# Performance work log

Measured on AMD Instinct MI355X. Metric: run time of the kernel, lower is better.

The kernel has to match this reference:

```python
import jax, jax.numpy as jnp
import numpy as np

B, C, K, D = 8192, 64, 256, 64  # batch, ncodebooks, ncentroids, subvect_len
BN_EPS = 1e-5


def setup_inputs() -> dict:
    key = jax.random.key(0)
    k1, k2 = jax.random.split(key)
    return {
        "inputs": jax.random.normal(k1, (B, C, D), dtype=jnp.float32),
        "centroids_k": jax.random.normal(k2, (C, K, D), dtype=jnp.float32) * 0.1,
        "bn_gamma": jnp.ones((C,), dtype=jnp.float32),
        "bn_beta": jnp.zeros((C,), dtype=jnp.float32),
    }


def _response(inputs, centroids_k, bn_gamma, bn_beta):
    # dot-metric scores: (B, C, K)
    r = jnp.einsum('bcd,ckd->bck', inputs, centroids_k)
    # BatchNorm1d over channel dim C (training mode: biased batch stats over B and K)
    mean = r.mean(axis=(0, 2), keepdims=True)
    var = ((r - mean) ** 2).mean(axis=(0, 2), keepdims=True)
    r = (r - mean) * jax.lax.rsqrt(var + BN_EPS)
    return r * bn_gamma[None, :, None] + bn_beta[None, :, None]


def reference(inputs, centroids_k, bn_gamma, bn_beta):
    r = _response(inputs, centroids_k, bn_gamma, bn_beta)
    # torch.max(response, -1) -> (values, indices)
    mse = r.max(axis=-1)                 # (B, C)
    codes = jnp.argmax(r, axis=-1)       # (B, C) int
    # tie_in_n_out=True: _centroids_v is _centroids_k
    return codes, mse, centroids_k
```

## Files before the change

kernel.cpp:

```cpp
#include <hip/hip_runtime.h>

#define B_  8192
#define C_  64
#define K_  256
#define D_  64
#define NBT     2
#define ROWS_BT 512
#define GX  (B_ / (ROWS_BT * NBT))
#define BC_ (B_ * C_)
#define BN_EPS 1e-5

#define WCAP_C 1024
#define DELTA  2.5e-3f

typedef _Float16 f16x8 __attribute__((ext_vector_type(8)));
typedef float    f32x4 __attribute__((ext_vector_type(4)));

__device__ __forceinline__ int swz(int row, int dbyte) {
    return (row * 128 + dbyte) ^ ((row & 7) << 4);
}

__device__ __forceinline__ f16x8 cvt8(const float* p) {
    float4 u0 = *(const float4*)p;
    float4 u1 = *(const float4*)(p + 4);
    return (f16x8){(_Float16)u0.x, (_Float16)u0.y, (_Float16)u0.z, (_Float16)u0.w,
                   (_Float16)u1.x, (_Float16)u1.y, (_Float16)u1.z, (_Float16)u1.w};
}

#define MERGE2(B1, S1, B2, S2)                                              \
    {                                                                       \
        const float lo_ = fminf(B1, B2);                                    \
        B1 = fmaxf(B1, B2);                                                 \
        S1 = fmaxf(lo_, fmaxf(S1, S2));                                     \
    }

__global__ __launch_bounds__(64) void dpq_prep(
    const float* __restrict__ cent, float* __restrict__ csum,
    int* __restrict__ wcount)
{
    const int c = blockIdx.x, d = threadIdx.x;
    const float* g = cent + (size_t)c * K_ * D_ + d;
    float s = 0.f;
#pragma unroll 8
    for (int k = 0; k < K_; ++k) s += g[(size_t)k * D_];
    csum[c * D_ + d] = s;
    if (d == 0) wcount[c] = 0;
}

__global__ __launch_bounds__(512, 4) void dpq_mfma(
    const float* __restrict__ x,
    const float* __restrict__ cent,
    const float* __restrict__ gamma,
    const float* __restrict__ csum,
    float* __restrict__ out,
    float* __restrict__ part_sum,
    float* __restrict__ part_sq,
    int* __restrict__ wcount,
    int* __restrict__ worklist)
{
    __shared__ char lds[34816];
    const int c   = blockIdx.y;
    const int tid = threadIdx.x;
    const float sgn = (gamma[c] < 0.0f) ? -1.0f : 1.0f;

    {
        const int row = tid >> 1, half = tid & 1;
        const float* g = cent + ((size_t)c * K_ + row) * D_ + half * 32;
#pragma unroll
        for (int q = 0; q < 4; ++q) {
            float v[8];
#pragma unroll
            for (int j = 0; j < 8; ++j) v[j] = g[q * 8 + j] * sgn;
            f16x8 h = {(_Float16)v[0], (_Float16)v[1], (_Float16)v[2], (_Float16)v[3],
                       (_Float16)v[4], (_Float16)v[5], (_Float16)v[6], (_Float16)v[7]};
            *(f16x8*)(lds + swz(row, half * 64 + q * 16)) = h;
        }
    }
    if (tid < 128) {
        const int row = tid >> 3, q = tid & 7;
        f16x8 h = {0, 0, 0, 0, 0, 0, 0, 0};
        if (row == 0) {
            const float* cs = csum + c * D_ + q * 8;
#pragma unroll
            for (int j = 0; j < 8; ++j) h[j] = (_Float16)(cs[j] * sgn);
        }
        *(f16x8*)(lds + 32768 + swz(row, q * 16)) = h;
    }
    __syncthreads();

    const int wid = tid >> 6, lane = tid & 63;
    const int col = lane & 15, grp = lane >> 4;
    const unsigned g4 = (unsigned)(grp * 4);

    float taccs[4] = {0.f, 0.f, 0.f, 0.f};
    float taccq[4] = {0.f, 0.f, 0.f, 0.f};

    for (int bt = 0; bt < NBT; ++bt) {
        const int b0 = blockIdx.x * (ROWS_BT * NBT) + bt * ROWS_BT + wid * 64;

        f16x8 xfa[4], xfb[4];
        {
            const float* xb = x + ((size_t)(b0 + col) * C_ + c) * D_ + grp * 8;
            const size_t st16 = (size_t)16 * C_ * D_;
#pragma unroll
            for (int T = 0; T < 4; ++T) {
                xfa[T] = cvt8(xb + T * st16);
                xfb[T] = cvt8(xb + T * st16 + 32);
            }
        }

        float bestv[4], secv[4];
#pragma unroll
        for (int T = 0; T < 4; ++T) { bestv[T] = -3.4e38f; secv[T] = -3.4e38f; }

#pragma unroll 4
        for (int t = 0; t < 16; ++t) {
            const f16x8 a0 = *(const f16x8*)(lds + swz(t * 16 + col,      grp * 16));
            const f16x8 a1 = *(const f16x8*)(lds + swz(t * 16 + col, 64 + grp * 16));

            f32x4 p[4];
#pragma unroll
            for (int T = 0; T < 4; ++T) {
                f32x4 acc = {0.f, 0.f, 0.f, 0.f};
                acc = __builtin_amdgcn_mfma_f32_16x16x32_f16(a0, xfa[T], acc, 0, 0, 0);
                acc = __builtin_amdgcn_mfma_f32_16x16x32_f16(a1, xfb[T], acc, 0, 0, 0);
                p[T] = acc;
            }

            const unsigned kt = ((unsigned)t << 4) | g4;
#pragma unroll
            for (int j = 0; j < 4; ++j) {
                const unsigned kj = kt + j;
#pragma unroll
                for (int T = 0; T < 4; ++T) {
                    const float r = p[T][j];
                    taccq[T] = fmaf(r, r, taccq[T]);
                    const float pk = __uint_as_float(
                        (__float_as_uint(r) & 0xFFFFFF00u) | kj);
                    secv[T]  = __builtin_amdgcn_fmed3f(pk, bestv[T], secv[T]);
                    bestv[T] = fmaxf(bestv[T], pk);
                }
            }
        }

        {
            const f16x8 a0v = *(const f16x8*)(lds + 32768 + swz(col,      grp * 16));
            const f16x8 a1v = *(const f16x8*)(lds + 32768 + swz(col, 64 + grp * 16));
#pragma unroll
            for (int T = 0; T < 4; ++T) {
                f32x4 pv = {0.f, 0.f, 0.f, 0.f};
                pv = __builtin_amdgcn_mfma_f32_16x16x32_f16(a0v, xfa[T], pv, 0, 0, 0);
                pv = __builtin_amdgcn_mfma_f32_16x16x32_f16(a1v, xfb[T], pv, 0, 0, 0);
                taccs[T] += pv[0];
            }
        }

#pragma unroll
        for (int T = 0; T < 4; ++T) {
            float bv = bestv[T], sv = secv[T];
#pragma unroll
            for (int m = 16; m <= 32; m <<= 1) {
                const float ob = __shfl_xor(bv, m);
                const float os = __shfl_xor(sv, m);
                MERGE2(bv, sv, ob, os);
            }
            if (grp == 0) {
                const int b = b0 + T * 16 + col;
                const size_t idx = (size_t)b * C_ + c;
                const unsigned bits = __float_as_uint(bv);
                out[idx] = (float)(bits & 255u);
                out[(size_t)BC_ + idx] = __uint_as_float(bits & 0xFFFFFF00u);
                if (bv - sv < DELTA && worklist) {
                    const int slot = atomicAdd(&wcount[c], 1);
                    if (slot < WCAP_C) worklist[c * WCAP_C + slot] = b;
                }
            }
        }
    }

    float accs = (taccs[0] + taccs[1]) + (taccs[2] + taccs[3]);
    float accq = (taccq[0] + taccq[1]) + (taccq[2] + taccq[3]);
#pragma unroll
    for (int m = 1; m <= 32; m <<= 1) {
        accs += __shfl_xor(accs, m);
        accq += __shfl_xor(accq, m);
    }
    __syncthreads();
    float* red = (float*)lds;
    if (lane == 0) { red[wid] = accs; red[8 + wid] = accq; }
    __syncthreads();
    if (tid == 0) {
        float s = 0.f, q = 0.f;
#pragma unroll
        for (int w = 0; w < 8; ++w) { s += red[w]; q += red[8 + w]; }
        part_sum[c * GX + blockIdx.x] = s;
        part_sq [c * GX + blockIdx.x] = q;
    }
}

__global__ __launch_bounds__(256) void dpq_referee(
    const float* __restrict__ x,
    const float* __restrict__ cent,
    const float* __restrict__ gamma,
    const int* __restrict__ wcount,
    const int* __restrict__ worklist,
    float* __restrict__ out)
{
    __shared__ float cl[K_ * D_];
    const int c = blockIdx.x;
    int n = wcount[c];
    if (n > WCAP_C) n = WCAP_C;
    if (n <= 0) return;
    const int t = threadIdx.x;
    const float sgnf = (gamma[c] < 0.0f) ? -1.0f : 1.0f;

    {
        const float* g = cent + ((size_t)c * K_ + t) * D_;
#pragma unroll 8
        for (int d = 0; d < D_; ++d)
            cl[t * D_ + (d ^ (t & 31))] = g[d];
    }
    __syncthreads();

    const int wid = t >> 6, lane = t & 63;
    for (int i = blockIdx.y * 4 + wid; i < n; i += gridDim.y * 4) {
        const int b = worklist[c * WCAP_C + i];
        const float* xr = x + ((size_t)b * C_ + c) * D_;
        double bv = -1.0e300;
        int bk = 0;
#pragma unroll
        for (int q = 0; q < 4; ++q) {
            const int k = q * 64 + lane;
            const int sw = k & 31;
            double s = 0.0;
#pragma unroll 8
            for (int d = 0; d < D_; ++d)
                s += (double)xr[d] * (double)cl[k * D_ + (d ^ sw)];
            s *= (double)sgnf;
            if (s > bv) { bv = s; bk = k; }
        }
#pragma unroll
        for (int m = 1; m <= 32; m <<= 1) {
            const double ov = __shfl_xor(bv, m);
            const int   ok = __shfl_xor(bk, m);
            if (ov > bv || (ov == bv && ok < bk)) { bv = ov; bk = ok; }
        }
        if (lane == 0) {
            const size_t idx = (size_t)b * C_ + c;
            out[idx] = (float)bk;
            out[(size_t)BC_ + idx] = (float)bv;
        }
    }
}

__global__ __launch_bounds__(256) void dpq_apply(
    float* __restrict__ out,
    const float* __restrict__ part_sum,
    const float* __restrict__ part_sq,
    const float* __restrict__ gamma,
    const float* __restrict__ beta,
    const float* __restrict__ cent)
{
    __shared__ float sc_s[C_], sh_s[C_];
    const int tid = threadIdx.x;
    if (tid < C_) {
        double s = 0.0, q = 0.0;
#pragma unroll
        for (int i = 0; i < GX; ++i) {
            s += (double)part_sum[tid * GX + i];
            q += (double)part_sq [tid * GX + i];
        }
        const double n    = (double)B_ * (double)K_;
        const double mean = s / n;
        const double var  = q / n - mean * mean;
        const double sc   = fabs((double)gamma[tid]) / sqrt(var + BN_EPS);
        sc_s[tid] = (float)sc;
        sh_s[tid] = (float)((double)beta[tid] - mean * sc);
    }
    __syncthreads();

    const int idx = blockIdx.x * 256 + tid;
    const int c = idx & (C_ - 1);
    const float sc = sc_s[c];
    const float sh = sh_s[c];
    if (sc == 0.0f) {
        out[idx] = 0.0f;
        out[(size_t)BC_ + idx] = sh;
    } else {
        out[(size_t)BC_ + idx] = fmaf(out[(size_t)BC_ + idx], sc, sh);
    }

    if (idx < (C_ * K_ * D_) / 4) {
        ((float4*)(out + 2 * (size_t)BC_))[idx] = ((const float4*)cent)[idx];
    }
}

extern "C" void kernel_launch(void* const* d_in, const int* in_sizes, int n_in,
                              void* d_out, int out_size, void* d_ws, size_t ws_size,
                              hipStream_t stream)
{
    const float* x     = (const float*)d_in[0];
    const float* cent  = (const float*)d_in[1];
    const float* gamma = (const float*)d_in[2];
    const float* beta  = (const float*)d_in[3];
    float* out = (float*)d_out;
    float* ws  = (float*)d_ws;

    float* csum     = ws;
    float* part_sum = ws + 4096;
    float* part_sq  = ws + 4608;
    int*   wcount   = (int*)(ws + 5120);
    int*   worklist = (int*)(ws + 5184);

    hipLaunchKernelGGL(dpq_prep, dim3(C_), dim3(64), 0, stream,
                       cent, csum, wcount);
    dim3 g1(GX, C_);
    hipLaunchKernelGGL(dpq_mfma, g1, dim3(512), 0, stream,
                       x, cent, gamma, csum, out, part_sum, part_sq,
                       wcount, worklist);
    hipLaunchKernelGGL(dpq_referee, dim3(C_, 4), dim3(256), 0, stream,
                       x, cent, gamma, wcount, worklist, out);
    hipLaunchKernelGGL(dpq_apply, dim3(BC_ / 256), dim3(256), 0, stream,
                       out, part_sum, part_sq, gamma, beta, cent);
}
```

Measured before the change: 100.6 us.

## Drop per-block batch-tile loop, double grid, split centroid-sum prep across threads

The main MFMA kernel no longer loops over two 512-row batch tiles per block. Each block now handles one tile, which doubles the grid in the batch dimension, and launch bounds rise to 6 blocks per SIMD-group target. The MFMA result is now consumed per T right after it is computed rather than buffered across all four tiles, which lowers register pressure. The prep kernel splits the 256-centroid column sum across 4 wavefronts and combines them through LDS, and the workspace offsets grow to hold twice as many partial statistics. The cost is that each block stages the centroids into LDS once for half as many rows, so total LDS fill work doubles.

```diff
diff --git a/kernel.cpp b/kernel.cpp
--- a/kernel.cpp
+++ b/kernel.cpp
@@ -4,9 +4,8 @@
 #define C_  64
 #define K_  256
 #define D_  64
-#define NBT     2
-#define ROWS_BT 512
-#define GX  (B_ / (ROWS_BT * NBT))
+#define WROWS 64
+#define GX  (B_ / (8 * WROWS))
 #define BC_ (B_ * C_)
 #define BN_EPS 1e-5
 
@@ -34,20 +33,25 @@
         S1 = fmaxf(lo_, fmaxf(S1, S2));                                     \
     }
 
-__global__ __launch_bounds__(64) void dpq_prep(
+__global__ __launch_bounds__(256) void dpq_prep(
     const float* __restrict__ cent, float* __restrict__ csum,
     int* __restrict__ wcount)
 {
-    const int c = blockIdx.x, d = threadIdx.x;
-    const float* g = cent + (size_t)c * K_ * D_ + d;
+    __shared__ float pacc[4][D_];
+    const int c = blockIdx.x, t = threadIdx.x;
+    const int d = t & 63, seg = t >> 6;
+    const float* g = cent + (size_t)c * K_ * D_ + (size_t)seg * 64 * D_ + d;
     float s = 0.f;
 #pragma unroll 8
-    for (int k = 0; k < K_; ++k) s += g[(size_t)k * D_];
-    csum[c * D_ + d] = s;
-    if (d == 0) wcount[c] = 0;
-}
-
-__global__ __launch_bounds__(512, 4) void dpq_mfma(
+    for (int k = 0; k < 64; ++k) s += g[(size_t)k * D_];
+    pacc[seg][d] = s;
+    __syncthreads();
+    if (t < D_)
+        csum[c * D_ + t] = (pacc[0][t] + pacc[1][t]) + (pacc[2][t] + pacc[3][t]);
+    if (t == 0) wcount[c] = 0;
+}
+
+__global__ __launch_bounds__(512, 6) void dpq_mfma(
     const float* __restrict__ x,
     const float* __restrict__ cent,
     const float* __restrict__ gamma,
@@ -91,89 +95,78 @@
     const int wid = tid >> 6, lane = tid & 63;
     const int col = lane & 15, grp = lane >> 4;
     const unsigned g4 = (unsigned)(grp * 4);
+    const int b0 = blockIdx.x * (8 * WROWS) + wid * WROWS;
+
+    f16x8 xfa[4], xfb[4];
+    {
+        const float* xb = x + ((size_t)(b0 + col) * C_ + c) * D_ + grp * 8;
+        const size_t st16 = (size_t)16 * C_ * D_;
+#pragma unroll
+        for (int T = 0; T < 4; ++T) {
+            xfa[T] = cvt8(xb + T * st16);
+            xfb[T] = cvt8(xb + T * st16 + 32);
+        }
+    }
 
     float taccs[4] = {0.f, 0.f, 0.f, 0.f};
     float taccq[4] = {0.f, 0.f, 0.f, 0.f};
-
-    for (int bt = 0; bt < NBT; ++bt) {
-        const int b0 = blockIdx.x * (ROWS_BT * NBT) + bt * ROWS_BT + wid * 64;
-
-        f16x8 xfa[4], xfb[4];
-        {
-            const float* xb = x + ((size_t)(b0 + col) * C_ + c) * D_ + grp * 8;
-            const size_t st16 = (size_t)16 * C_ * D_;
-#pragma unroll
-            for (int T = 0; T < 4; ++T) {
-                xfa[T] = cvt8(xb + T * st16);
-                xfb[T] = cvt8(xb + T * st16 + 32);
+    float bestv[4], secv[4];
+#pragma unroll
+    for (int T = 0; T < 4; ++T) { bestv[T] = -3.4e38f; secv[T] = -3.4e38f; }
+
+#pragma unroll 4
+    for (int t = 0; t < 16; ++t) {
+        const f16x8 a0 = *(const f16x8*)(lds + swz(t * 16 + col,      grp * 16));
+        const f16x8 a1 = *(const f16x8*)(lds + swz(t * 16 + col, 64 + grp * 16));
+        const unsigned kt = ((unsigned)t << 4) | g4;
+
+#pragma unroll
+        for (int T = 0; T < 4; ++T) {
+            f32x4 acc = {0.f, 0.f, 0.f, 0.f};
+            acc = __builtin_amdgcn_mfma_f32_16x16x32_f16(a0, xfa[T], acc, 0, 0, 0);
+            acc = __builtin_amdgcn_mfma_f32_16x16x32_f16(a1, xfb[T], acc, 0, 0, 0);
+#pragma unroll
+            for (int j = 0; j < 4; ++j) {
+                const float r = acc[j];
+                taccq[T] = fmaf(r, r, taccq[T]);
+                const float pk = __uint_as_float(
+                    (__float_as_uint(r) & 0xFFFFFF00u) | (kt + j));
+                secv[T]  = __builtin_amdgcn_fmed3f(pk, bestv[T], secv[T]);
+                bestv[T] = fmaxf(bestv[T], pk);
             }
         }
-
-        float bestv[4], secv[4];
-#pragma unroll
-        for (int T = 0; T < 4; ++T) { bestv[T] = -3.4e38f; secv[T] = -3.4e38f; }
-
-#pragma unroll 4
-        for (int t = 0; t < 16; ++t) {
-            const f16x8 a0 = *(const f16x8*)(lds + swz(t * 16 + col,      grp * 16));
-            const f16x8 a1 = *(const f16x8*)(lds + swz(t * 16 + col, 64 + grp * 16));
-
-            f32x4 p[4];
-#pragma unroll
-            for (int T = 0; T < 4; ++T) {
-                f32x4 acc = {0.f, 0.f, 0.f, 0.f};
-                acc = __builtin_amdgcn_mfma_f32_16x16x32_f16(a0, xfa[T], acc, 0, 0, 0);
-                acc = __builtin_amdgcn_mfma_f32_16x16x32_f16(a1, xfb[T], acc, 0, 0, 0);
-                p[T] = acc;
-            }
-
-            const unsigned kt = ((unsigned)t << 4) | g4;
-#pragma unroll
-            for (int j = 0; j < 4; ++j) {
-                const unsigned kj = kt + j;
-#pragma unroll
-                for (int T = 0; T < 4; ++T) {
-                    const float r = p[T][j];
-                    taccq[T] = fmaf(r, r, taccq[T]);
-                    const float pk = __uint_as_float(
-                        (__float_as_uint(r) & 0xFFFFFF00u) | kj);
-                    secv[T]  = __builtin_amdgcn_fmed3f(pk, bestv[T], secv[T]);
-                    bestv[T] = fmaxf(bestv[T], pk);
-                }
-            }
-        }
-
-        {
-            const f16x8 a0v = *(const f16x8*)(lds + 32768 + swz(col,      grp * 16));
-            const f16x8 a1v = *(const f16x8*)(lds + 32768 + swz(col, 64 + grp * 16));
-#pragma unroll
-            for (int T = 0; T < 4; ++T) {
-                f32x4 pv = {0.f, 0.f, 0.f, 0.f};
-                pv = __builtin_amdgcn_mfma_f32_16x16x32_f16(a0v, xfa[T], pv, 0, 0, 0);
-                pv = __builtin_amdgcn_mfma_f32_16x16x32_f16(a1v, xfb[T], pv, 0, 0, 0);
-                taccs[T] += pv[0];
-            }
-        }
-
+    }
+
+    {
+        const f16x8 a0v = *(const f16x8*)(lds + 32768 + swz(col,      grp * 16));
+        const f16x8 a1v = *(const f16x8*)(lds + 32768 + swz(col, 64 + grp * 16));
 #pragma unroll
         for (int T = 0; T < 4; ++T) {
-            float bv = bestv[T], sv = secv[T];
-#pragma unroll
-            for (int m = 16; m <= 32; m <<= 1) {
-                const float ob = __shfl_xor(bv, m);
-                const float os = __shfl_xor(sv, m);
-                MERGE2(bv, sv, ob, os);
-            }
-            if (grp == 0) {
-                const int b = b0 + T * 16 + col;
-                const size_t idx = (size_t)b * C_ + c;
-                const unsigned bits = __float_as_uint(bv);
-                out[idx] = (float)(bits & 255u);
-                out[(size_t)BC_ + idx] = __uint_as_float(bits & 0xFFFFFF00u);
-                if (bv - sv < DELTA && worklist) {
-                    const int slot = atomicAdd(&wcount[c], 1);
-                    if (slot < WCAP_C) worklist[c * WCAP_C + slot] = b;
-                }
+            f32x4 pv = {0.f, 0.f, 0.f, 0.f};
+            pv = __builtin_amdgcn_mfma_f32_16x16x32_f16(a0v, xfa[T], pv, 0, 0, 0);
+            pv = __builtin_amdgcn_mfma_f32_16x16x32_f16(a1v, xfb[T], pv, 0, 0, 0);
+            taccs[T] += pv[0];
+        }
+    }
+
+#pragma unroll
+    for (int T = 0; T < 4; ++T) {
+        float bv = bestv[T], sv = secv[T];
+#pragma unroll
+        for (int m = 16; m <= 32; m <<= 1) {
+            const float ob = __shfl_xor(bv, m);
+            const float os = __shfl_xor(sv, m);
+            MERGE2(bv, sv, ob, os);
+        }
+        if (grp == 0) {
+            const int b = b0 + T * 16 + col;
+            const size_t idx = (size_t)b * C_ + c;
+            const unsigned bits = __float_as_uint(bv);
+            out[idx] = (float)(bits & 255u);
+            out[(size_t)BC_ + idx] = __uint_as_float(bits & 0xFFFFFF00u);
+            if (bv - sv < DELTA) {
+                const int slot = atomicAdd(&wcount[c], 1);
+                if (slot < WCAP_C) worklist[c * WCAP_C + slot] = b;
             }
         }
     }
@@ -308,11 +301,11 @@
 
     float* csum     = ws;
     float* part_sum = ws + 4096;
-    float* part_sq  = ws + 4608;
-    int*   wcount   = (int*)(ws + 5120);
-    int*   worklist = (int*)(ws + 5184);
-
-    hipLaunchKernelGGL(dpq_prep, dim3(C_), dim3(64), 0, stream,
+    float* part_sq  = ws + 5120;
+    int*   wcount   = (int*)(ws + 6144);
+    int*   worklist = (int*)(ws + 6208);
+
+    hipLaunchKernelGGL(dpq_prep, dim3(C_), dim3(256), 0, stream,
                        cent, csum, wcount);
     dim3 g1(GX, C_);
     hipLaunchKernelGGL(dpq_mfma, g1, dim3(512), 0, stream,
```

Measured after the change: 109.4 us. 1.09x slower.
